# Performance work log

Hardware: AMD Instinct MI355X
Metric: run time of the kernel (lower is better)

Reference implementation:

```python
import jax, jax.numpy as jnp
import numpy as np

STATE_DIM, ACTION_DIM, HIDDEN_DIM = 512, 64, 2048
INPUT_DIM = STATE_DIM + ACTION_DIM + 1  # 577
BATCH = 4096


def setup_inputs() -> dict:
    key = jax.random.key(0)
    ks = jax.random.split(key, 12)
    sc_x = 1.0 / np.sqrt(INPUT_DIM)
    sc_h = 1.0 / np.sqrt(HIDDEN_DIM)
    return {
        "s": jax.random.normal(ks[0], (BATCH, STATE_DIM), jnp.float32),
        "a_prev": jax.random.normal(ks[1], (BATCH, ACTION_DIM), jnp.float32),
        "r_prev": jax.random.normal(ks[2], (BATCH, 1), jnp.float32),
        "h": jnp.zeros((HIDDEN_DIM,), jnp.float32),
        "c": jnp.zeros((HIDDEN_DIM,), jnp.float32),
        # Fused gate weights: columns ordered [i, f, g(c-tilde), o]
        "Wx": jax.random.uniform(ks[3], (INPUT_DIM, 4 * HIDDEN_DIM), jnp.float32, -sc_x, sc_x),
        "Wh": jax.random.uniform(ks[4], (HIDDEN_DIM, 4 * HIDDEN_DIM), jnp.float32, -sc_h, sc_h),
        "bh": jax.random.uniform(ks[5], (4 * HIDDEN_DIM,), jnp.float32, -sc_h, sc_h),
        "Wa": jax.random.uniform(ks[6], (HIDDEN_DIM, ACTION_DIM), jnp.float32, -sc_h, sc_h),
        "ba": jax.random.uniform(ks[7], (ACTION_DIM,), jnp.float32, -sc_h, sc_h),
        "Wv": jax.random.uniform(ks[8], (HIDDEN_DIM, 1), jnp.float32, -sc_h, sc_h),
        "bv": jax.random.uniform(ks[9], (1,), jnp.float32, -sc_h, sc_h),
    }


def reference(s, a_prev, r_prev, h, c, Wx, Wh, bh, Wa, ba, Wv, bv):
    # x: [B, input_dim]
    x = jnp.concatenate([s, a_prev, r_prev], axis=1)
    # Two fused GEMMs replace the 8 separate small linears (same math).
    z = x @ Wx + h @ Wh + bh          # [B, 4H]
    zi, zf, zg, zo = jnp.split(z, 4, axis=-1)
    i = jax.nn.sigmoid(zi)
    f = jax.nn.sigmoid(zf)
    c_new = f * c + i * jnp.tanh(zg)  # [B, H] (c broadcast over batch)
    o = jax.nn.sigmoid(zo)
    h_new = o * jnp.tanh(c_new)       # [B, H]
    probs = jax.nn.softmax(h_new @ Wa + ba, axis=1)  # [B, A]
    v = h_new @ Wv + bv               # [B, 1]
    return (probs, v)
```

## Files before the change

### kernel.cpp

```cpp
#include <hip/hip_runtime.h>
#include <hip/hip_bf16.h>

#define BATCH   4096
#define SDIM    512
#define ADIM    64
#define IDIM    577
#define KP2     640
#define NKT64   10
#define HDIM    2048
#define ZDIM    8192
#define BUFE    (128 * 64)

typedef __attribute__((ext_vector_type(8))) __bf16 bf16x8;
typedef __attribute__((ext_vector_type(4))) float  accx4;

__global__ __launch_bounds__(256) void setup_kernel(
    const float* __restrict__ s, const float* __restrict__ a_prev,
    const float* __restrict__ r_prev, const float* __restrict__ h,
    const float* __restrict__ wx, const float* __restrict__ wh,
    const float* __restrict__ wa,
    __hip_bfloat16* __restrict__ xb, __hip_bfloat16* __restrict__ wxt,
    __hip_bfloat16* __restrict__ waT, float* __restrict__ zh_w)
{
    __shared__ float stile[64 * 65];
    const int bid = blockIdx.x;
    const int t = threadIdx.x;

    if (bid < 1280) {
        const int kt2 = bid >> 7;
        const int nt  = bid & 127;
        const int c4  = t & 15;
        const int rr  = t >> 4;
#pragma unroll
        for (int i = 0; i < 4; ++i) {
            const int r = rr + i * 16;
            const int k = kt2 * 64 + r;
            float4 v = (k < IDIM)
                ? *(const float4*)(wx + (size_t)k * ZDIM + nt * 64 + c4 * 4)
                : float4{0.f, 0.f, 0.f, 0.f};
            *(float4*)(stile + r * 65 + c4 * 4) = v;
        }
        __syncthreads();
        const int ch = t & 7;
#pragma unroll
        for (int i = 0; i < 2; ++i) {
            const int nr = (t >> 3) + i * 32;
            bf16x8 w8;
#pragma unroll
            for (int j = 0; j < 8; ++j)
                w8[j] = (__bf16)stile[(ch * 8 + j) * 65 + nr];
            *(bf16x8*)(wxt + (size_t)(nt * 64 + nr) * KP2 + kt2 * 64 + ch * 8)
                = w8;
        }
    } else if (bid < 1536) {
        const int zb = bid - 1280;
        const int nb = zb & 31, ky = zb >> 5;
        const int n  = nb * 256 + t;
        const float* hp  = h + ky * 256;
        const float* whp = wh + (size_t)ky * 256 * ZDIM + n;
        float p = 0.0f;
#pragma unroll 16
        for (int kk = 0; kk < 256; ++kk)
            p = fmaf(hp[kk], whp[(size_t)kk * ZDIM], p);
        zh_w[ky * ZDIM + n] = p;
    } else if (bid < 5632) {
        const int row = bid - 1536;
        const float* srow = s + (size_t)row * SDIM;
        const float* arow = a_prev + (size_t)row * ADIM;
        __hip_bfloat16* xrow = xb + (size_t)row * KP2;
        for (int c = t; c < KP2; c += 256) {
            float v;
            if (c < SDIM)        v = srow[c];
            else if (c < 576)    v = arow[c - SDIM];
            else if (c == 576)   v = r_prev[row];
            else                 v = 0.0f;
            xrow[c] = __float2bfloat16(v);
        }
    } else {
        const int wb = bid - 5632;
        const int kt = wb >> 1, at = wb & 1;
        const int c  = t & 31, r0 = t >> 5;
#pragma unroll
        for (int i = 0; i < 4; ++i) {
            int r = r0 + i * 8;
            stile[r * 33 + c] = wa[(size_t)(kt * 32 + r) * ADIM + at * 32 + c];
        }
        __syncthreads();
#pragma unroll
        for (int i = 0; i < 4; ++i) {
            int r = r0 + i * 8;
            waT[(size_t)(at * 32 + r) * HDIM + kt * 32 + c] =
                __float2bfloat16(stile[c * 33 + r]);
        }
    }
}

__device__ __forceinline__ float sigmoid_f(float x) {
    return 1.0f / (1.0f + __expf(-x));
}
__device__ __forceinline__ float tanh_f(float x) {
    return 1.0f - 2.0f / (1.0f + __expf(2.0f * x));
}

__global__ __launch_bounds__(256, 2) void lstm_gemm(
    const __hip_bfloat16* __restrict__ xb,
    const __hip_bfloat16* __restrict__ wxt,
    const float* __restrict__ zh_w,
    const float* __restrict__ bh,
    const float* __restrict__ cvec,
    __hip_bfloat16* __restrict__ hout)
{
    __shared__ __bf16 smA[2 * BUFE];
    __shared__ __bf16 smB[2 * BUFE];
    const int t    = threadIdx.x;
    const int lane = t & 63;
    const int wid  = t >> 6;
    const int m0   = blockIdx.x * 128;
    const int n0   = blockIdx.y * 32;
    const int wm   = wid >> 1, wn = wid & 1;
    const int fl15 = lane & 15;
    const int fhi  = lane >> 4;

    accx4 acc[4][4] = {};

    const int srow = lane >> 3;
    const int slot = lane & 7;
    const int cch  = slot ^ srow;
    const __bf16* gA[4]; const __bf16* gB[4]; int lofs[4];
#pragma unroll
    for (int i = 0; i < 4; ++i) {
        const int r = wid * 32 + i * 8 + srow;
        gA[i] = (const __bf16*)xb + (size_t)(m0 + r) * KP2 + cch * 8;
        const int g = r >> 5, nn = r & 31;
        gB[i] = (const __bf16*)wxt +
                (size_t)(g * HDIM + n0 + nn) * KP2 + cch * 8;
        lofs[i] = (wid * 32 + i * 8) * 64;
    }

    auto stage = [&](int tile, int p) {
        const int ko = tile * 64;
        const int po = p * BUFE;
#pragma unroll
        for (int i = 0; i < 4; ++i) {
            __builtin_amdgcn_global_load_lds(
                (const __attribute__((address_space(1))) void*)(gA[i] + ko),
                (__attribute__((address_space(3))) void*)(smA + po + lofs[i]),
                16, 0, 0);
            __builtin_amdgcn_global_load_lds(
                (const __attribute__((address_space(1))) void*)(gB[i] + ko),
                (__attribute__((address_space(3))) void*)(smB + po + lofs[i]),
                16, 0, 0);
        }
    };

    auto compute = [&](int p) {
        const int po = p * BUFE;
#pragma unroll
        for (int hf = 0; hf < 2; ++hf) {
            const int ck = hf * 4 + fhi;
            const int sl = (ck ^ (fl15 & 7)) * 8;
            bf16x8 af[4], bfr[4];
#pragma unroll
            for (int rt = 0; rt < 4; ++rt)
                af[rt] = *(const bf16x8*)(smA + po +
                    (wm * 64 + rt * 16 + fl15) * 64 + sl);
#pragma unroll
            for (int g = 0; g < 4; ++g)
                bfr[g] = *(const bf16x8*)(smB + po +
                    (g * 32 + wn * 16 + fl15) * 64 + sl);
#pragma unroll
            for (int g = 0; g < 4; ++g)
#pragma unroll
                for (int rt = 0; rt < 4; ++rt)
                    acc[g][rt] = __builtin_amdgcn_mfma_f32_16x16x32_bf16(
                        af[rt], bfr[g], acc[g][rt], 0, 0, 0);
        }
    };

    stage(0, 0);
    __syncthreads();
#pragma unroll
    for (int kt = 0; kt < NKT64 - 1; ++kt) {
        stage(kt + 1, (kt + 1) & 1);
        compute(kt & 1);
        __syncthreads();
    }
    compute((NKT64 - 1) & 1);

    const int colg = n0 + wn * 16 + fl15;
    float zsum[4];
#pragma unroll
    for (int g = 0; g < 4; ++g) {
        float z = bh[g * HDIM + colg];
#pragma unroll
        for (int j = 0; j < 8; ++j)
            z += zh_w[j * ZDIM + g * HDIM + colg];
        zsum[g] = z;
    }
    const float cv = cvec[colg];
#pragma unroll
    for (int rt = 0; rt < 4; ++rt) {
#pragma unroll
        for (int r = 0; r < 4; ++r) {
            const int row = m0 + wm * 64 + rt * 16 + (fhi << 2) + r;
            const float zi = acc[0][rt][r] + zsum[0];
            const float zf = acc[1][rt][r] + zsum[1];
            const float zg = acc[2][rt][r] + zsum[2];
            const float zo = acc[3][rt][r] + zsum[3];
            const float cn = sigmoid_f(zf) * cv + sigmoid_f(zi) * tanh_f(zg);
            const float hn = sigmoid_f(zo) * tanh_f(cn);
            hout[(size_t)row * HDIM + colg] = __float2bfloat16(hn);
        }
    }
}

__global__ __launch_bounds__(512) void head_kernel(
    const __hip_bfloat16* __restrict__ hnew,
    const __hip_bfloat16* __restrict__ waT,
    const float* __restrict__ wv,
    const float* __restrict__ ba, const float* __restrict__ bv,
    float* __restrict__ probs, float* __restrict__ vout)
{
    __shared__ float lg[8][16][68];
    __shared__ float vpart[8][16];
    const int t    = threadIdx.x;
    const int lane = t & 63;
    const int w    = t >> 6;
    const int r0   = blockIdx.x * 16;
    const int fl15 = lane & 15, fhi = lane >> 4;
    const int k0   = w * 256;

    const __bf16* arow = (const __bf16*)hnew +
        (size_t)(r0 + fl15) * HDIM + k0 + fhi * 8;
    const __bf16* brow = (const __bf16*)waT +
        (size_t)fl15 * HDIM + k0 + fhi * 8;
    const float* wvp = wv + k0 + fhi * 8;

    accx4 acc[4] = {};
    float va0 = 0.f, va1 = 0.f;
#pragma unroll
    for (int kk = 0; kk < 256; kk += 32) {
        bf16x8 af = *(const bf16x8*)(arow + kk);
#pragma unroll
        for (int a = 0; a < 4; ++a) {
            bf16x8 bf = *(const bf16x8*)(brow + (size_t)a * 16 * HDIM + kk);
            acc[a] = __builtin_amdgcn_mfma_f32_16x16x32_bf16(
                af, bf, acc[a], 0, 0, 0);
        }
#pragma unroll
        for (int j = 0; j < 4; ++j) {
            va0 = fmaf((float)af[j],     wvp[kk + j],     va0);
            va1 = fmaf((float)af[j + 4], wvp[kk + j + 4], va1);
        }
    }
#pragma unroll
    for (int a = 0; a < 4; ++a)
#pragma unroll
        for (int r = 0; r < 4; ++r)
            lg[w][fhi * 4 + r][a * 16 + fl15] = acc[a][r];
    float va = va0 + va1;
    va += __shfl_xor(va, 16);
    va += __shfl_xor(va, 32);
    if (lane < 16) vpart[w][lane] = va;
    __syncthreads();

    const float bav = ba[lane];
#pragma unroll
    for (int i = 0; i < 2; ++i) {
        const int row = w * 2 + i;
        float logit = bav;
#pragma unroll
        for (int p = 0; p < 8; ++p)
            logit += lg[p][row][lane];
        float m = logit;
#pragma unroll
        for (int mask = 32; mask >= 1; mask >>= 1)
            m = fmaxf(m, __shfl_xor(m, mask));
        const float e = __expf(logit - m);
        float ssum = e;
#pragma unroll
        for (int mask = 32; mask >= 1; mask >>= 1)
            ssum += __shfl_xor(ssum, mask);
        probs[(size_t)(r0 + row) * 64 + lane] = e / ssum;
    }
    if (t < 16) {
        float v = bv[0];
#pragma unroll
        for (int p = 0; p < 8; ++p)
            v += vpart[p][t];
        vout[r0 + t] = v;
    }
}

extern "C" void kernel_launch(void* const* d_in, const int* in_sizes, int n_in,
                              void* d_out, int out_size, void* d_ws,
                              size_t ws_size, hipStream_t stream)
{
    const float* s      = (const float*)d_in[0];
    const float* a_prev = (const float*)d_in[1];
    const float* r_prev = (const float*)d_in[2];
    const float* h      = (const float*)d_in[3];
    const float* c      = (const float*)d_in[4];
    const float* Wx     = (const float*)d_in[5];
    const float* Wh     = (const float*)d_in[6];
    const float* bh     = (const float*)d_in[7];
    const float* Wa     = (const float*)d_in[8];
    const float* ba     = (const float*)d_in[9];
    const float* Wv     = (const float*)d_in[10];
    const float* bv     = (const float*)d_in[11];

    float* out   = (float*)d_out;
    float* probs = out;
    float* vout  = out + (size_t)BATCH * ADIM;

    char* ws = (char*)d_ws;
    __hip_bfloat16* xb   = (__hip_bfloat16*)ws;
    __hip_bfloat16* wxt  = (__hip_bfloat16*)(ws + 5242880);
    __hip_bfloat16* waT  = (__hip_bfloat16*)(ws + 15728640);
    float* zh_w          = (float*)(ws + 15990784);
    __hip_bfloat16* hnew = (__hip_bfloat16*)(ws + 16252928);

    setup_kernel<<<5760, 256, 0, stream>>>(
        s, a_prev, r_prev, h, Wx, Wh, Wa, xb, wxt, waT, zh_w);
    lstm_gemm<<<dim3(BATCH / 128, HDIM / 32), 256, 0, stream>>>(
        xb, wxt, zh_w, bh, c, hnew);
    head_kernel<<<BATCH / 16, 512, 0, stream>>>(
        hnew, waT, Wv, ba, bv, probs, vout);
}
```

Before: 212.7 us.

## Drop padded K tile by folding r_prev column into epilogue; split h@Wh finer

Input K is shrunk from 640 to 576 by moving the single r_prev column out of the bf16 GEMM and applying it as a rank-1 fp32 update in the gate epilogue, which removes one of ten K tiles in the main GEMM and the zero-padding work in setup. The h@Wh matvec is split into 16 partial chunks instead of 8 to expose more parallelism, so the epilogue now sums 16 partials. Sigmoid and tanh use a hardware reciprocal instead of a division. Costs are extra per-element loads of r_prev and Wx row 576 in the epilogue and slightly lower precision from the approximate reciprocal.

```diff
diff --git a/kernel.cpp b/kernel.cpp
--- a/kernel.cpp
+++ b/kernel.cpp
@@ -5,8 +5,8 @@
 #define SDIM    512
 #define ADIM    64
 #define IDIM    577
-#define KP2     640
-#define NKT64   10
+#define KP2     576
+#define NKT64   9
 #define HDIM    2048
 #define ZDIM    8192
 #define BUFE    (128 * 64)
@@ -16,7 +16,7 @@
 
 __global__ __launch_bounds__(256) void setup_kernel(
     const float* __restrict__ s, const float* __restrict__ a_prev,
-    const float* __restrict__ r_prev, const float* __restrict__ h,
+    const float* __restrict__ h,
     const float* __restrict__ wx, const float* __restrict__ wh,
     const float* __restrict__ wa,
     __hip_bfloat16* __restrict__ xb, __hip_bfloat16* __restrict__ wxt,
@@ -26,7 +26,7 @@
     const int bid = blockIdx.x;
     const int t = threadIdx.x;
 
-    if (bid < 1280) {
+    if (bid < 1152) {
         const int kt2 = bid >> 7;
         const int nt  = bid & 127;
         const int c4  = t & 15;
@@ -35,9 +35,8 @@
         for (int i = 0; i < 4; ++i) {
             const int r = rr + i * 16;
             const int k = kt2 * 64 + r;
-            float4 v = (k < IDIM)
-                ? *(const float4*)(wx + (size_t)k * ZDIM + nt * 64 + c4 * 4)
-                : float4{0.f, 0.f, 0.f, 0.f};
+            float4 v =
+                *(const float4*)(wx + (size_t)k * ZDIM + nt * 64 + c4 * 4);
             *(float4*)(stile + r * 65 + c4 * 4) = v;
         }
         __syncthreads();
@@ -52,32 +51,28 @@
             *(bf16x8*)(wxt + (size_t)(nt * 64 + nr) * KP2 + kt2 * 64 + ch * 8)
                 = w8;
         }
-    } else if (bid < 1536) {
-        const int zb = bid - 1280;
+    } else if (bid < 1664) {
+        const int zb = bid - 1152;
         const int nb = zb & 31, ky = zb >> 5;
         const int n  = nb * 256 + t;
-        const float* hp  = h + ky * 256;
-        const float* whp = wh + (size_t)ky * 256 * ZDIM + n;
+        const float* hp  = h + ky * 128;
+        const float* whp = wh + (size_t)ky * 128 * ZDIM + n;
         float p = 0.0f;
-#pragma unroll 16
-        for (int kk = 0; kk < 256; ++kk)
+#pragma unroll 32
+        for (int kk = 0; kk < 128; ++kk)
             p = fmaf(hp[kk], whp[(size_t)kk * ZDIM], p);
         zh_w[ky * ZDIM + n] = p;
-    } else if (bid < 5632) {
-        const int row = bid - 1536;
+    } else if (bid < 5760) {
+        const int row = bid - 1664;
         const float* srow = s + (size_t)row * SDIM;
         const float* arow = a_prev + (size_t)row * ADIM;
         __hip_bfloat16* xrow = xb + (size_t)row * KP2;
         for (int c = t; c < KP2; c += 256) {
-            float v;
-            if (c < SDIM)        v = srow[c];
-            else if (c < 576)    v = arow[c - SDIM];
-            else if (c == 576)   v = r_prev[row];
-            else                 v = 0.0f;
+            const float v = (c < SDIM) ? srow[c] : arow[c - SDIM];
             xrow[c] = __float2bfloat16(v);
         }
     } else {
-        const int wb = bid - 5632;
+        const int wb = bid - 5760;
         const int kt = wb >> 1, at = wb & 1;
         const int c  = t & 31, r0 = t >> 5;
 #pragma unroll
@@ -95,11 +90,14 @@
     }
 }
 
+__device__ __forceinline__ float rcp_f(float x) {
+    return __builtin_amdgcn_rcpf(x);
+}
 __device__ __forceinline__ float sigmoid_f(float x) {
-    return 1.0f / (1.0f + __expf(-x));
+    return rcp_f(1.0f + __expf(-x));
 }
 __device__ __forceinline__ float tanh_f(float x) {
-    return 1.0f - 2.0f / (1.0f + __expf(2.0f * x));
+    return 1.0f - 2.0f * rcp_f(1.0f + __expf(2.0f * x));
 }
 
 __global__ __launch_bounds__(256, 2) void lstm_gemm(
@@ -108,6 +106,8 @@
     const float* __restrict__ zh_w,
     const float* __restrict__ bh,
     const float* __restrict__ cvec,
+    const float* __restrict__ wx,
+    const float* __restrict__ r_prev,
     __hip_bfloat16* __restrict__ hout)
 {
     __shared__ __bf16 smA[2 * BUFE];
@@ -188,14 +188,15 @@
     compute((NKT64 - 1) & 1);
 
     const int colg = n0 + wn * 16 + fl15;
-    float zsum[4];
+    float zsum[4], wxr[4];
 #pragma unroll
     for (int g = 0; g < 4; ++g) {
         float z = bh[g * HDIM + colg];
 #pragma unroll
-        for (int j = 0; j < 8; ++j)
+        for (int j = 0; j < 16; ++j)
             z += zh_w[j * ZDIM + g * HDIM + colg];
         zsum[g] = z;
+        wxr[g] = wx[(size_t)576 * ZDIM + g * HDIM + colg];
     }
     const float cv = cvec[colg];
 #pragma unroll
@@ -203,10 +204,11 @@
 #pragma unroll
         for (int r = 0; r < 4; ++r) {
             const int row = m0 + wm * 64 + rt * 16 + (fhi << 2) + r;
-            const float zi = acc[0][rt][r] + zsum[0];
-            const float zf = acc[1][rt][r] + zsum[1];
-            const float zg = acc[2][rt][r] + zsum[2];
-            const float zo = acc[3][rt][r] + zsum[3];
+            const float rv = r_prev[row];
+            const float zi = acc[0][rt][r] + zsum[0] + rv * wxr[0];
+            const float zf = acc[1][rt][r] + zsum[1] + rv * wxr[1];
+            const float zg = acc[2][rt][r] + zsum[2] + rv * wxr[2];
+            const float zo = acc[3][rt][r] + zsum[3] + rv * wxr[3];
             const float cn = sigmoid_f(zf) * cv + sigmoid_f(zi) * tanh_f(zg);
             const float hn = sigmoid_f(zo) * tanh_f(cn);
             hout[(size_t)row * HDIM + colg] = __float2bfloat16(hn);
@@ -315,15 +317,15 @@
 
     char* ws = (char*)d_ws;
     __hip_bfloat16* xb   = (__hip_bfloat16*)ws;
-    __hip_bfloat16* wxt  = (__hip_bfloat16*)(ws + 5242880);
-    __hip_bfloat16* waT  = (__hip_bfloat16*)(ws + 15728640);
-    float* zh_w          = (float*)(ws + 15990784);
-    __hip_bfloat16* hnew = (__hip_bfloat16*)(ws + 16252928);
-
-    setup_kernel<<<5760, 256, 0, stream>>>(
-        s, a_prev, r_prev, h, Wx, Wh, Wa, xb, wxt, waT, zh_w);
+    __hip_bfloat16* wxt  = (__hip_bfloat16*)(ws + 4718592);
+    __hip_bfloat16* waT  = (__hip_bfloat16*)(ws + 14155776);
+    float* zh_w          = (float*)(ws + 14417920);
+    __hip_bfloat16* hnew = (__hip_bfloat16*)(ws + 14942208);
+
+    setup_kernel<<<5888, 256, 0, stream>>>(
+        s, a_prev, h, Wx, Wh, Wa, xb, wxt, waT, zh_w);
     lstm_gemm<<<dim3(BATCH / 128, HDIM / 32), 256, 0, stream>>>(
-        xb, wxt, zh_w, bh, c, hnew);
+        xb, wxt, zh_w, bh, c, Wx, r_prev, hnew);
     head_kernel<<<BATCH / 16, 512, 0, stream>>>(
         hnew, waT, Wv, ba, bv, probs, vout);
 }
```

After: 204.6 us. 3.8% less time.
